# Kernel tuning notes

Hardware: AMD Instinct MI355X
Metric: run time of the kernel (lower is better)

## Reference

```python
import jax, jax.numpy as jnp
import numpy as np

N, H, D = 65536, 8, 32      # n_points, num_heads, dim_per_head (h_dim)
CD = 3                      # coords_dim
NW = 3                      # num_w_per_dist
BS = 128                    # block_size
NH = 2                      # n_hashes


def layer_norm(x, g, b, eps=1e-5):
    mu = x.mean(-1, keepdims=True)
    var = ((x - mu) ** 2).mean(-1, keepdims=True)
    return (x - mu) * jax.lax.rsqrt(var + eps) * g + b


def hept_attn(q, k, v, pe, Wrpe):
    """HEPT-style LSH-sorted block-diagonal attention with relative-position kernel.
    q,k,v: (N,H,D); pe: (N,CD); Wrpe: (NW*(CD-1), H*D) (w_rpe.weight^T).
    score_ij = q_i.k_j/sqrt(D) - sum_r omega[h,r]*(p_i,r - p_j,r)^2 within LSH blocks.
    """
    # per-head, per-distance-dim nonnegative RPE weights derived from w_rpe.weight
    omega = (Wrpe.T.reshape(H, D, CD - 1, NW) ** 2).mean(axis=(1, 3))  # (H, CD-1)
    # E2LSH-style random projections of coordinates -> NH scalar hash codes
    proj = jax.random.normal(jax.random.key(42), (NH, CD), dtype=q.dtype)
    codes = pe @ proj.T  # (N, NH)
    scale = 1.0 / jnp.sqrt(jnp.asarray(D, q.dtype))
    nb = N // BS
    out = jnp.zeros((N, H * D), dtype=q.dtype)
    for r in range(NH):
        order = jnp.argsort(codes[:, r])
        inv = jnp.argsort(order)
        qs = q[order].reshape(nb, BS, H, D)
        ks = k[order].reshape(nb, BS, H, D)
        vs = v[order].reshape(nb, BS, H, D)
        ps = pe[order][:, : CD - 1].reshape(nb, BS, CD - 1)
        scores = jnp.einsum("bqhd,bkhd->bhqk", qs, ks) * scale      # (nb,H,BS,BS)
        diff2 = (ps[:, :, None, :] - ps[:, None, :, :]) ** 2        # (nb,BS,BS,CD-1)
        scores = scores - jnp.einsum("hr,bqkr->bhqk", omega, diff2)
        attn = jax.nn.softmax(scores, axis=-1)
        o = jnp.einsum("bhqk,bkhd->bqhd", attn, vs).reshape(N, H * D)
        out = out + o[inv]
    return out / NH


def setup_inputs() -> dict:
    key = jax.random.key(0)
    ks = jax.random.split(key, 16)
    s = 0.02
    return {
        "x": jax.random.normal(ks[0], (N, D), jnp.float32),
        "coords": jax.random.uniform(ks[1], (N, CD), jnp.float32),
        "g1": jnp.ones((D,), jnp.float32),
        "be1": jnp.zeros((D,), jnp.float32),
        "Wq": jax.random.normal(ks[2], (D, H * D), jnp.float32) * s,
        "Wk": jax.random.normal(ks[3], (D, H * D), jnp.float32) * s,
        "Wv": jax.random.normal(ks[4], (D, H * D), jnp.float32) * s,
        "Wrpe": jax.random.normal(ks[5], (NW * (CD - 1), H * D), jnp.float32) * s,
        "Wo": jax.random.normal(ks[6], (H * D, D), jnp.float32) * s,
        "bo": jnp.zeros((D,), jnp.float32),
        "g2": jnp.ones((D,), jnp.float32),
        "be2": jnp.zeros((D,), jnp.float32),
        "W1": jax.random.normal(ks[7], (D, D), jnp.float32) * s,
        "b1": jnp.zeros((D,), jnp.float32),
        "W2": jax.random.normal(ks[8], (D, D), jnp.float32) * s,
        "b2": jnp.zeros((D,), jnp.float32),
    }


def reference(x, coords, g1, be1, Wq, Wk, Wv, Wrpe, Wo, bo, g2, be2, W1, b1, W2, b2):
    # pe_type == 'none' -> pe = coords, x_pe = x (no additive PE)
    xn = layer_norm(x, g1, be1)
    q = (xn @ Wq).reshape(N, H, D)
    k = (xn @ Wk).reshape(N, H, D)
    v = (xn @ Wv).reshape(N, H, D)
    aggr = hept_attn(q, k, v, coords, Wrpe)
    x = x + aggr @ Wo + bo                       # residual (dropout = identity, eval)
    h = layer_norm(x, g2, be2)
    ff = jax.nn.relu(h @ W1 + b1) @ W2 + b2
    return x + ff
```

## Files before the change

### kernel.cpp

```cpp
#include <hip/hip_runtime.h>
#include <stdint.h>

typedef uint32_t u32;
typedef unsigned long long u64;
typedef unsigned short ushort;
typedef __attribute__((ext_vector_type(8))) short short8;
typedef __attribute__((ext_vector_type(4))) float f32x4;

#define NPTS 65536
#define HEADS 8
#define DIM 32
#define HD 256
#define BSZ 128
#define NBLK 512
#define SCALE_QK 0.17677669529663687f
#define LOG2E 1.4426950408889634f

__device__ __forceinline__ u32 rotl32(u32 v, int r){ return (v << r) | (v >> (32 - r)); }

__device__ void threefry2x32_0_42(u32 x0, u32 x1, u32& o0, u32& o1){
  const u32 ks0 = 0u, ks1 = 42u;
  const u32 ks2 = ks0 ^ ks1 ^ 0x1BD11BDAu;
  x0 += ks0; x1 += ks1;
#define TF_RND(r) { x0 += x1; x1 = rotl32(x1, (r)); x1 ^= x0; }
  TF_RND(13) TF_RND(15) TF_RND(26) TF_RND(6)
  x0 += ks1; x1 += ks2 + 1u;
  TF_RND(17) TF_RND(29) TF_RND(16) TF_RND(24)
  x0 += ks2; x1 += ks0 + 2u;
  TF_RND(13) TF_RND(15) TF_RND(26) TF_RND(6)
  x0 += ks0; x1 += ks1 + 3u;
  TF_RND(17) TF_RND(29) TF_RND(16) TF_RND(24)
  x0 += ks1; x1 += ks2 + 4u;
  TF_RND(13) TF_RND(15) TF_RND(26) TF_RND(6)
  x0 += ks2; x1 += ks0 + 5u;
#undef TF_RND
  o0 = x0; o1 = x1;
}

__device__ float erfinv_xla_f32(float x){
  float w = -log1pf(-x * x);
  float p;
  if (w < 5.0f){
    w = w - 2.5f;
    p =            2.81022636e-08f;
    p = fmaf(p, w, 3.43273939e-07f);
    p = fmaf(p, w, -3.5233877e-06f);
    p = fmaf(p, w, -4.39150654e-06f);
    p = fmaf(p, w,  0.00021858087f);
    p = fmaf(p, w, -0.00125372503f);
    p = fmaf(p, w, -0.00417768164f);
    p = fmaf(p, w,  0.246640727f);
    p = fmaf(p, w,  1.50140941f);
  } else {
    w = sqrtf(w) - 3.0f;
    p =            -0.000200214257f;
    p = fmaf(p, w,  0.000100950558f);
    p = fmaf(p, w,  0.00134934322f);
    p = fmaf(p, w, -0.00367342844f);
    p = fmaf(p, w,  0.00573950773f);
    p = fmaf(p, w, -0.0076224613f);
    p = fmaf(p, w,  0.00943887047f);
    p = fmaf(p, w,  1.00167406f);
    p = fmaf(p, w,  2.83297682f);
  }
  return p * x;
}

__device__ float jax_normal_from_bits(u32 bits){
  float f = __uint_as_float((bits >> 9) | 0x3f800000u) - 1.0f;
  const float mn = -0.99999994f;
  float v = fmaf(f, 2.0f, mn);
  v = fmaxf(mn, v);
  return 1.41421356237309505f * erfinv_xla_f32(v);
}

__device__ __forceinline__ ushort f2bf(float f){
  union { __bf16 b; ushort u; } cv;
  cv.b = (__bf16)f;
  return cv.u;
}

__global__ __launch_bounds__(1024) void k_sort2048(const float* __restrict__ coords,
                                                   const float* __restrict__ Wrpe,
                                                   const float* __restrict__ x,
                                                   const float* __restrict__ g1,
                                                   const float* __restrict__ be1,
                                                   float* __restrict__ omega,
                                                   ushort* __restrict__ xn,
                                                   u64* __restrict__ A0, u64* __restrict__ A1){
  __shared__ u64 sh[2048];
  int t = threadIdx.x;
  int bb = blockIdx.x;
  int r = (bb >= 32);
  u64* A = r ? A1 : A0;
  int base = (bb & 31) * 2048;

  {
    int gt = bb*1024 + t;
    const float4* xp = (const float4*)(x + (size_t)gt*32);
    float mu = 0.f, s2 = 0.f;
    #pragma unroll
    for (int c4 = 0; c4 < 8; c4++){
      float4 f = xp[c4];
      mu += f.x + f.y + f.z + f.w;
      s2 = fmaf(f.x,f.x, fmaf(f.y,f.y, fmaf(f.z,f.z, fmaf(f.w,f.w, s2))));
    }
    mu *= (1.0f/32.0f);
    float var = fmaf(-mu, mu, s2*(1.0f/32.0f));
    float rs = rsqrtf(var + 1e-5f);
    #pragma unroll
    for (int c4 = 0; c4 < 8; c4++){
      float4 f = xp[c4];
      u32 w0 = (u32)f2bf((f.x-mu)*rs*g1[c4*4+0] + be1[c4*4+0])
             | ((u32)f2bf((f.y-mu)*rs*g1[c4*4+1] + be1[c4*4+1]) << 16);
      u32 w1 = (u32)f2bf((f.z-mu)*rs*g1[c4*4+2] + be1[c4*4+2])
             | ((u32)f2bf((f.w-mu)*rs*g1[c4*4+3] + be1[c4*4+3]) << 16);
      *(uint2*)&xn[(size_t)gt*32 + c4*4] = make_uint2(w0, w1);
    }
  }

  float pr[3];
  #pragma unroll
  for (int j = 0; j < 3; j++){
    u32 a, b;
    threefry2x32_0_42((u32)j, (u32)(j + 3), a, b);
    pr[j] = jax_normal_from_bits(r ? b : a);
  }
  #pragma unroll
  for (int half = 0; half < 2; half++){
    int idx = base + t + half*1024;
    float c0 = coords[idx*3+0], c1 = coords[idx*3+1], c2 = coords[idx*3+2];
    float code = fmaf(c2, pr[2], fmaf(c1, pr[1], c0*pr[0]));
    u32 u = __float_as_uint(code);
    u32 key = (u & 0x80000000u) ? ~u : (u | 0x80000000u);
    sh[t + half*1024] = ((u64)key << 32) | (u64)(u32)idx;
  }
  __syncthreads();
  for (int k = 2; k <= 2048; k <<= 1){
    for (int j = k >> 1; j > 0; j >>= 1){
      int idx = ((t & ~(j-1)) << 1) | (t & (j-1));
      int par = idx | j;
      bool up = ((idx & k) == 0);
      u64 a = sh[idx], b = sh[par];
      if ((a > b) == up){ sh[idx] = b; sh[par] = a; }
      __syncthreads();
    }
  }
  A[base + t] = sh[t];
  A[base + t + 1024] = sh[t + 1024];

  if (bb == 0 && t < 16){
    int h = t >> 1, rr = t & 1;
    float s = 0.f;
    for (int wi = 0; wi < 3; wi++)
      for (int d = 0; d < 32; d++){
        float w = Wrpe[(rr*3 + wi)*HD + h*32 + d];
        s = fmaf(w, w, s);
      }
    omega[t] = s * (1.0f/96.0f);
  }
}

template<int NRG>
__global__ void k_merge2(const u64* __restrict__ s0, const u64* __restrict__ s1,
                         u64* __restrict__ d0, u64* __restrict__ d1, int lgL){
  int gb = blockIdx.x;
  const u64* src = (gb < 256) ? s0 : s1;
  u64*       dst = (gb < 256) ? d0 : d1;
  int g = (gb & 255) * 256 + threadIdx.x;
  int L = 1 << lgL;
  u64 e = src[g];
  int myrun = (g >> lgL) & (NRG - 1);
  int gbase = g & ~(NRG*L - 1);
  int pos = g & (L - 1);
  #pragma unroll
  for (int o = 0; o < NRG; o++){
    if (o == myrun) continue;
    const u64* run = src + gbase + o*L;
    int lo = 0, hi = L;
    while (lo < hi){
      int mid = (lo + hi) >> 1;
      if (run[mid] < e) lo = mid + 1; else hi = mid;
    }
    pos += lo;
  }
  dst[gbase + pos] = e;
}

__global__ __launch_bounds__(256, 4) void k_attn(const u64* __restrict__ s0,
    const u64* __restrict__ s1,
    const ushort* __restrict__ xn, const float* __restrict__ coords,
    const float* __restrict__ Wq, const float* __restrict__ Wk, const float* __restrict__ Wv,
    const float* __restrict__ omega, ushort* __restrict__ ag0, ushort* __restrict__ ag1){
  __shared__ __align__(16) char smem[38400];
  ushort* Xs = (ushort*)(smem + 0);
  ushort* Wt = (ushort*)(smem + 10240);
  ushort* Ps = (ushort*)(smem + 0);
  ushort* Ks = (ushort*)(smem + 17920);
  ushort* Vt = (ushort*)(smem + 28160);
  int*    gq_s = (int*)(smem + 36864);
  float2* ps_s = (float2*)(smem + 37376);
  ushort* Qs = Xs;

  const int bid = blockIdx.x;
  const int h = bid >> 10;
  const int b = (bid >> 1) & 511;
  const int r = bid & 1;
  const u64* sorted = r ? s1 : s0;
  ushort* aggr = r ? ag1 : ag0;

  const int t = threadIdx.x;
  const int w = t >> 6, l = t & 63, lg = l >> 4, lc = l & 15;
  const int R = w * 32;

  if (t < 128){
    int gp = (int)(u32)(sorted[b*BSZ + t] & 0xffffffffull);
    gq_s[t] = gp;
    float2 pc; pc.x = coords[gp*3+0]; pc.y = coords[gp*3+1];
    ps_s[t] = pc;
    const uint4* xr = (const uint4*)(xn + (size_t)gp*32);
    #pragma unroll
    for (int q4 = 0; q4 < 4; q4++)
      *(uint4*)&Xs[t*40 + q4*8] = xr[q4];
  } else {
    int tt = t - 128;
    #pragma unroll
    for (int e = 0; e < 24; e++){
      int flat = tt + e*128;
      int c  = (flat >> 5) & 31;
      int dl = flat & 31;
      const float* Wm = (e < 8) ? Wq : (e < 16) ? Wk : Wv;
      int m = e >> 3;
      float wv_ = Wm[c*HD + h*32 + dl];
      if (e < 8) wv_ *= SCALE_QK * LOG2E;
      Wt[(m*32 + dl)*40 + c] = f2bf(wv_);
    }
  }
  __syncthreads();

  {
    short8 a0 = *(const short8*)&Xs[(R      + lc)*40 + lg*8];
    short8 a1 = *(const short8*)&Xs[(R + 16 + lc)*40 + lg*8];
    short8 wq0 = *(const short8*)&Wt[(     lc)*40 + lg*8];
    short8 wq1 = *(const short8*)&Wt[(16 + lc)*40 + lg*8];
    f32x4 qtc[2][2];
    qtc[0][0] = __builtin_amdgcn_mfma_f32_16x16x32_bf16(wq0, a0, (f32x4){0.f,0.f,0.f,0.f}, 0, 0, 0);
    qtc[0][1] = __builtin_amdgcn_mfma_f32_16x16x32_bf16(wq0, a1, (f32x4){0.f,0.f,0.f,0.f}, 0, 0, 0);
    qtc[1][0] = __builtin_amdgcn_mfma_f32_16x16x32_bf16(wq1, a0, (f32x4){0.f,0.f,0.f,0.f}, 0, 0, 0);
    qtc[1][1] = __builtin_amdgcn_mfma_f32_16x16x32_bf16(wq1, a1, (f32x4){0.f,0.f,0.f,0.f}, 0, 0, 0);
    #pragma unroll
    for (int ct = 2; ct < 6; ct++){
      short8 bb = *(const short8*)&Wt[(ct*16 + lc)*40 + lg*8];
      f32x4 d0 = __builtin_amdgcn_mfma_f32_16x16x32_bf16(a0, bb, (f32x4){0.f,0.f,0.f,0.f}, 0, 0, 0);
      f32x4 d1 = __builtin_amdgcn_mfma_f32_16x16x32_bf16(a1, bb, (f32x4){0.f,0.f,0.f,0.f}, 0, 0, 0);
      #pragma unroll
      for (int i = 0; i < 4; i++){
        int r0 = R + lg*4 + i, r1 = r0 + 16;
        if (ct < 4){
          Ks[r0*40 + (ct-2)*16 + lc] = f2bf(d0[i]);
          Ks[r1*40 + (ct-2)*16 + lc] = f2bf(d1[i]);
        } else {
          Vt[((ct-4)*16 + lc)*136 + r0] = f2bf(d0[i]);
          Vt[((ct-4)*16 + lc)*136 + r1] = f2bf(d1[i]);
        }
      }
    }
    #pragma unroll
    for (int qt = 0; qt < 2; qt++)
      #pragma unroll
      for (int dt = 0; dt < 2; dt++){
        u32 w0 = (u32)f2bf(qtc[dt][qt][0]) | ((u32)f2bf(qtc[dt][qt][1]) << 16);
        u32 w1 = (u32)f2bf(qtc[dt][qt][2]) | ((u32)f2bf(qtc[dt][qt][3]) << 16);
        *(uint2*)&Qs[(R + qt*16 + lc)*40 + dt*16 + lg*4] = make_uint2(w0, w1);
      }
  }
  __syncthreads();

  short8 bq[2];
  bq[0] = *(const short8*)&Qs[(R      + lc)*40 + lg*8];
  bq[1] = *(const short8*)&Qs[(R + 16 + lc)*40 + lg*8];

  const float om0 = omega[h*2+0] * LOG2E, om1 = omega[h*2+1] * LOG2E;
  short8 bAug[2];
  #pragma unroll
  for (int qt = 0; qt < 2; qt++){
    float2 pq = ps_s[R + qt*16 + lc];
    u32 wrd[4];
    wrd[0] = (lg == 0) ? ((u32)f2bf(2.0f*om0*pq.x) | ((u32)f2bf(2.0f*om1*pq.y) << 16)) : 0u;
    wrd[1] = (lg == 0) ? (u32)f2bf(1.0f) : 0u;
    wrd[2] = 0u; wrd[3] = 0u;
    bAug[qt] = *(short8*)&wrd[0];
  }

  f32x4 acc[2][8];
  #pragma unroll
  for (int kt = 0; kt < 8; kt++){
    short8 ak = *(const short8*)&Ks[(kt*16 + lc)*40 + lg*8];
    float2 pk = ps_s[kt*16 + lc];
    float nK = -fmaf(om0, pk.x*pk.x, om1*(pk.y*pk.y));
    u32 wrd[4];
    wrd[0] = (lg == 0) ? ((u32)f2bf(pk.x) | ((u32)f2bf(pk.y) << 16)) : 0u;
    wrd[1] = (lg == 0) ? (u32)f2bf(nK) : 0u;
    wrd[2] = 0u; wrd[3] = 0u;
    short8 aAug = *(short8*)&wrd[0];
    acc[0][kt] = __builtin_amdgcn_mfma_f32_16x16x32_bf16(ak, bq[0], (f32x4){0.f,0.f,0.f,0.f}, 0, 0, 0);
    acc[1][kt] = __builtin_amdgcn_mfma_f32_16x16x32_bf16(ak, bq[1], (f32x4){0.f,0.f,0.f,0.f}, 0, 0, 0);
    acc[0][kt] = __builtin_amdgcn_mfma_f32_16x16x32_bf16(aAug, bAug[0], acc[0][kt], 0, 0, 0);
    acc[1][kt] = __builtin_amdgcn_mfma_f32_16x16x32_bf16(aAug, bAug[1], acc[1][kt], 0, 0, 0);
  }

  float lr[2] = {0.f, 0.f};
  #pragma unroll
  for (int qt = 0; qt < 2; qt++)
    #pragma unroll
    for (int kt = 0; kt < 8; kt++)
      #pragma unroll
      for (int i = 0; i < 4; i++){
        float e = exp2f(acc[qt][kt][i]);
        acc[qt][kt][i] = e;
        lr[qt] += e;
      }
  #pragma unroll
  for (int qt = 0; qt < 2; qt++){
    float s = lr[qt];
    s += __shfl_xor(s, 16);
    s += __shfl_xor(s, 32);
    lr[qt] = 0.5f / s;
  }

  short8 av[4][2];
  #pragma unroll
  for (int cc = 0; cc < 4; cc++)
    #pragma unroll
    for (int dt = 0; dt < 2; dt++)
      av[cc][dt] = *(const short8*)&Vt[(dt*16 + lc)*136 + cc*32 + lg*8];

  __syncthreads();

  ushort* Psw = Ps + w*16*136;
  f32x4 oT[2][2];
  #pragma unroll
  for (int dt = 0; dt < 2; dt++)
    #pragma unroll
    for (int qt = 0; qt < 2; qt++) oT[dt][qt] = (f32x4){0.f,0.f,0.f,0.f};

  #pragma unroll
  for (int qt = 0; qt < 2; qt++){
    asm volatile("s_waitcnt lgkmcnt(0)" ::: "memory");
    __builtin_amdgcn_sched_barrier(0);
    #pragma unroll
    for (int kt = 0; kt < 8; kt++){
      u32 p0 = (u32)f2bf(acc[qt][kt][0]) | ((u32)f2bf(acc[qt][kt][1]) << 16);
      u32 p1 = (u32)f2bf(acc[qt][kt][2]) | ((u32)f2bf(acc[qt][kt][3]) << 16);
      *(uint2*)&Psw[lc*136 + kt*16 + lg*4] = make_uint2(p0, p1);
    }
    asm volatile("s_waitcnt lgkmcnt(0)" ::: "memory");
    __builtin_amdgcn_sched_barrier(0);
    __builtin_amdgcn_s_setprio(1);
    #pragma unroll
    for (int cc = 0; cc < 4; cc++){
      short8 bp = *(const short8*)&Psw[lc*136 + cc*32 + lg*8];
      oT[0][qt] = __builtin_amdgcn_mfma_f32_16x16x32_bf16(av[cc][0], bp, oT[0][qt], 0, 0, 0);
      oT[1][qt] = __builtin_amdgcn_mfma_f32_16x16x32_bf16(av[cc][1], bp, oT[1][qt], 0, 0, 0);
    }
    __builtin_amdgcn_s_setprio(0);
  }

  #pragma unroll
  for (int qt = 0; qt < 2; qt++){
    int g = gq_s[R + qt*16 + lc];
    float lrq = lr[qt];
    ushort* dst = aggr + (size_t)g*HD + h*32;
    #pragma unroll
    for (int dt = 0; dt < 2; dt++){
      u32 w0 = (u32)f2bf(oT[dt][qt][0]*lrq) | ((u32)f2bf(oT[dt][qt][1]*lrq) << 16);
      u32 w1 = (u32)f2bf(oT[dt][qt][2]*lrq) | ((u32)f2bf(oT[dt][qt][3]*lrq) << 16);
      *(uint2*)&dst[dt*16 + lg*4] = make_uint2(w0, w1);
    }
  }
}

__global__ __launch_bounds__(256) void k_out(const float* __restrict__ x,
    const ushort* __restrict__ ag0, const ushort* __restrict__ ag1,
    const float* __restrict__ Wo, const float* __restrict__ bo,
    const float* __restrict__ g2, const float* __restrict__ be2,
    const float* __restrict__ W1, const float* __restrict__ b1,
    const float* __restrict__ W2, const float* __restrict__ b2,
    float* __restrict__ out){
  __shared__ ushort Wot[32*264];
  __shared__ ushort W1t[32*40];
  __shared__ ushort W2t[32*40];
  __shared__ ushort Bnc[4][16*40];
  int t = threadIdx.x;
  #pragma unroll
  for (int e = 0; e < 32; e++){
    int flat = t + e*256;
    int k = flat >> 5, col = flat & 31;
    Wot[col*264 + k] = f2bf(Wo[flat]);
  }
  #pragma unroll
  for (int e = 0; e < 4; e++){
    int flat = t + e*256;
    int k = flat >> 5, col = flat & 31;
    W1t[col*40 + k] = f2bf(W1[flat]);
    W2t[col*40 + k] = f2bf(W2[flat]);
  }
  __syncthreads();

  const int w = t >> 6, l = t & 63, lg = l >> 4, lc = l & 15;
  const int r0 = blockIdx.x*64 + w*16;

  f32x4 acc[2];
  acc[0] = (f32x4){0.f,0.f,0.f,0.f};
  acc[1] = (f32x4){0.f,0.f,0.f,0.f};
  #pragma unroll
  for (int ks = 0; ks < 8; ks++){
    short8 a0 = *(const short8*)(ag0 + (size_t)(r0+lc)*256 + ks*32 + lg*8);
    short8 a1 = *(const short8*)(ag1 + (size_t)(r0+lc)*256 + ks*32 + lg*8);
    #pragma unroll
    for (int ct = 0; ct < 2; ct++){
      short8 bb = *(const short8*)&Wot[(ct*16 + lc)*264 + ks*32 + lg*8];
      acc[ct] = __builtin_amdgcn_mfma_f32_16x16x32_bf16(a0, bb, acc[ct], 0, 0, 0);
      acc[ct] = __builtin_amdgcn_mfma_f32_16x16x32_bf16(a1, bb, acc[ct], 0, 0, 0);
    }
  }
  float x2v[2][4];
  #pragma unroll
  for (int ct = 0; ct < 2; ct++){
    int col = ct*16 + lc;
    float bov = bo[col];
    #pragma unroll
    for (int i = 0; i < 4; i++){
      int row = r0 + lg*4 + i;
      x2v[ct][i] = x[row*32 + col] + acc[ct][i] + bov;
    }
  }

  float g2v[2], be2v[2], b1v[2], b2v[2];
  #pragma unroll
  for (int ct = 0; ct < 2; ct++){
    int col = ct*16 + lc;
    g2v[ct] = g2[col]; be2v[ct] = be2[col]; b1v[ct] = b1[col]; b2v[ct] = b2[col];
  }
  ushort* B = &Bnc[w][0];
  #pragma unroll
  for (int i = 0; i < 4; i++){
    float m = x2v[0][i] + x2v[1][i];
    m += __shfl_xor(m, 1); m += __shfl_xor(m, 2);
    m += __shfl_xor(m, 4); m += __shfl_xor(m, 8);
    float mu = m * (1.0f/32.0f);
    float d0 = x2v[0][i] - mu, d1 = x2v[1][i] - mu;
    float v = fmaf(d0, d0, d1*d1);
    v += __shfl_xor(v, 1); v += __shfl_xor(v, 2);
    v += __shfl_xor(v, 4); v += __shfl_xor(v, 8);
    float rs = rsqrtf(v * (1.0f/32.0f) + 1e-5f);
    B[(lg*4 + i)*40 +      lc] = f2bf(d0 * rs * g2v[0] + be2v[0]);
    B[(lg*4 + i)*40 + 16 + lc] = f2bf(d1 * rs * g2v[1] + be2v[1]);
  }
  asm volatile("s_waitcnt lgkmcnt(0)" ::: "memory");
  __builtin_amdgcn_sched_barrier(0);

  short8 ha = *(const short8*)&B[lc*40 + lg*8];
  f32x4 f1[2];
  #pragma unroll
  for (int ct = 0; ct < 2; ct++){
    short8 bb = *(const short8*)&W1t[(ct*16 + lc)*40 + lg*8];
    f1[ct] = __builtin_amdgcn_mfma_f32_16x16x32_bf16(ha, bb, (f32x4){0.f,0.f,0.f,0.f}, 0, 0, 0);
  }
  asm volatile("s_waitcnt lgkmcnt(0)" ::: "memory");
  __builtin_amdgcn_sched_barrier(0);
  #pragma unroll
  for (int ct = 0; ct < 2; ct++)
    #pragma unroll
    for (int i = 0; i < 4; i++)
      B[(lg*4 + i)*40 + ct*16 + lc] = f2bf(fmaxf(f1[ct][i] + b1v[ct], 0.f));
  asm volatile("s_waitcnt lgkmcnt(0)" ::: "memory");
  __builtin_amdgcn_sched_barrier(0);

  short8 ta = *(const short8*)&B[lc*40 + lg*8];
  #pragma unroll
  for (int ct = 0; ct < 2; ct++){
    short8 bb = *(const short8*)&W2t[(ct*16 + lc)*40 + lg*8];
    f32x4 f2 = __builtin_amdgcn_mfma_f32_16x16x32_bf16(ta, bb, (f32x4){0.f,0.f,0.f,0.f}, 0, 0, 0);
    int col = ct*16 + lc;
    #pragma unroll
    for (int i = 0; i < 4; i++){
      int row = r0 + lg*4 + i;
      out[row*32 + col] = x2v[ct][i] + f2[i] + b2v[ct];
    }
  }
}

extern "C" void kernel_launch(void* const* d_in, const int* in_sizes, int n_in,
                              void* d_out, int out_size, void* d_ws, size_t ws_size,
                              hipStream_t stream) {
  (void)in_sizes; (void)n_in; (void)out_size; (void)ws_size;
  const float* x      = (const float*)d_in[0];
  const float* coords = (const float*)d_in[1];
  const float* g1     = (const float*)d_in[2];
  const float* be1    = (const float*)d_in[3];
  const float* Wq     = (const float*)d_in[4];
  const float* Wk     = (const float*)d_in[5];
  const float* Wv     = (const float*)d_in[6];
  const float* Wrpe   = (const float*)d_in[7];
  const float* Wo     = (const float*)d_in[8];
  const float* bo     = (const float*)d_in[9];
  const float* g2     = (const float*)d_in[10];
  const float* be2    = (const float*)d_in[11];
  const float* W1     = (const float*)d_in[12];
  const float* b1     = (const float*)d_in[13];
  const float* W2     = (const float*)d_in[14];
  const float* b2     = (const float*)d_in[15];
  float* out = (float*)d_out;

  char* ws = (char*)d_ws;
  ushort* ag0   = (ushort*)(ws + 0);
  ushort* ag1   = (ushort*)(ws + 33554432);
  ushort* xn    = (ushort*)(ws + 67108864);
  u64*   keyA0  = (u64*)  (ws + 71303168);
  u64*   keyA1  = (u64*)  (ws + 71827456);
  u64*   keyB0  = (u64*)  (ws + 72351744);
  u64*   keyB1  = (u64*)  (ws + 72876032);
  float* omega  = (float*)(ws + 73400320);

  k_sort2048<<<64, 1024, 0, stream>>>(coords, Wrpe, x, g1, be1, omega, xn, keyA0, keyA1);
  k_merge2<4><<<512, 256, 0, stream>>>(keyA0, keyA1, keyB0, keyB1, 11);
  k_merge2<4><<<512, 256, 0, stream>>>(keyB0, keyB1, keyA0, keyA1, 13);
  k_merge2<2><<<512, 256, 0, stream>>>(keyA0, keyA1, keyB0, keyB1, 15);

  k_attn<<<NBLK*HEADS*2, 256, 0, stream>>>(keyB0, keyB1, xn, coords,
                                           Wq, Wk, Wv, omega, ag0, ag1);

  k_out<<<NPTS/64, 256, 0, stream>>>(x, ag0, ag1, Wo, bo, g2, be2, W1, b1, W2, b2, out);
}
```

Before: 144.3 us.

## Shrink bitonic sort tiles to 1024 and compute K via transposed MFMA

The initial bitonic sort now sorts 1024-key tiles with 512-thread blocks on 128 blocks instead of 2048-key tiles on 64 blocks. The merge passes are re-parameterised so that three radix-4 merges cover the larger number of runs. Separately, the attention kernel now computes K with the weight as the A operand, the same way as Q. This lets K be written to shared memory with packed 8-byte stores instead of scattered 2-byte stores, and V stores are also packed. The aim is better GPU occupancy in the sort and fewer LDS store instructions in the QKV projection, in exchange for a final merge that is 4-way instead of 2-way.

```diff
diff --git a/kernel.cpp b/kernel.cpp
--- a/kernel.cpp
+++ b/kernel.cpp
@@ -80,23 +80,23 @@
   return cv.u;
 }
 
-__global__ __launch_bounds__(1024) void k_sort2048(const float* __restrict__ coords,
-                                                   const float* __restrict__ Wrpe,
-                                                   const float* __restrict__ x,
-                                                   const float* __restrict__ g1,
-                                                   const float* __restrict__ be1,
-                                                   float* __restrict__ omega,
-                                                   ushort* __restrict__ xn,
-                                                   u64* __restrict__ A0, u64* __restrict__ A1){
-  __shared__ u64 sh[2048];
+__global__ __launch_bounds__(512) void k_sort1024(const float* __restrict__ coords,
+                                                  const float* __restrict__ Wrpe,
+                                                  const float* __restrict__ x,
+                                                  const float* __restrict__ g1,
+                                                  const float* __restrict__ be1,
+                                                  float* __restrict__ omega,
+                                                  ushort* __restrict__ xn,
+                                                  u64* __restrict__ A0, u64* __restrict__ A1){
+  __shared__ u64 sh[1024];
   int t = threadIdx.x;
   int bb = blockIdx.x;
-  int r = (bb >= 32);
+  int r = (bb >= 64);
   u64* A = r ? A1 : A0;
-  int base = (bb & 31) * 2048;
+  int base = (bb & 63) * 1024;
 
   {
-    int gt = bb*1024 + t;
+    int gt = bb*512 + t;
     const float4* xp = (const float4*)(x + (size_t)gt*32);
     float mu = 0.f, s2 = 0.f;
     #pragma unroll
@@ -128,15 +128,15 @@
   }
   #pragma unroll
   for (int half = 0; half < 2; half++){
-    int idx = base + t + half*1024;
+    int idx = base + t + half*512;
     float c0 = coords[idx*3+0], c1 = coords[idx*3+1], c2 = coords[idx*3+2];
     float code = fmaf(c2, pr[2], fmaf(c1, pr[1], c0*pr[0]));
     u32 u = __float_as_uint(code);
     u32 key = (u & 0x80000000u) ? ~u : (u | 0x80000000u);
-    sh[t + half*1024] = ((u64)key << 32) | (u64)(u32)idx;
+    sh[t + half*512] = ((u64)key << 32) | (u64)(u32)idx;
   }
   __syncthreads();
-  for (int k = 2; k <= 2048; k <<= 1){
+  for (int k = 2; k <= 1024; k <<= 1){
     for (int j = k >> 1; j > 0; j >>= 1){
       int idx = ((t & ~(j-1)) << 1) | (t & (j-1));
       int par = idx | j;
@@ -147,7 +147,7 @@
     }
   }
   A[base + t] = sh[t];
-  A[base + t + 1024] = sh[t + 1024];
+  A[base + t + 512] = sh[t + 512];
 
   if (bb == 0 && t < 16){
     int h = t >> 1, rr = t & 1;
@@ -241,38 +241,40 @@
   {
     short8 a0 = *(const short8*)&Xs[(R      + lc)*40 + lg*8];
     short8 a1 = *(const short8*)&Xs[(R + 16 + lc)*40 + lg*8];
-    short8 wq0 = *(const short8*)&Wt[(     lc)*40 + lg*8];
-    short8 wq1 = *(const short8*)&Wt[(16 + lc)*40 + lg*8];
-    f32x4 qtc[2][2];
-    qtc[0][0] = __builtin_amdgcn_mfma_f32_16x16x32_bf16(wq0, a0, (f32x4){0.f,0.f,0.f,0.f}, 0, 0, 0);
-    qtc[0][1] = __builtin_amdgcn_mfma_f32_16x16x32_bf16(wq0, a1, (f32x4){0.f,0.f,0.f,0.f}, 0, 0, 0);
-    qtc[1][0] = __builtin_amdgcn_mfma_f32_16x16x32_bf16(wq1, a0, (f32x4){0.f,0.f,0.f,0.f}, 0, 0, 0);
-    qtc[1][1] = __builtin_amdgcn_mfma_f32_16x16x32_bf16(wq1, a1, (f32x4){0.f,0.f,0.f,0.f}, 0, 0, 0);
-    #pragma unroll
-    for (int ct = 2; ct < 6; ct++){
-      short8 bb = *(const short8*)&Wt[(ct*16 + lc)*40 + lg*8];
-      f32x4 d0 = __builtin_amdgcn_mfma_f32_16x16x32_bf16(a0, bb, (f32x4){0.f,0.f,0.f,0.f}, 0, 0, 0);
-      f32x4 d1 = __builtin_amdgcn_mfma_f32_16x16x32_bf16(a1, bb, (f32x4){0.f,0.f,0.f,0.f}, 0, 0, 0);
-      #pragma unroll
-      for (int i = 0; i < 4; i++){
-        int r0 = R + lg*4 + i, r1 = r0 + 16;
-        if (ct < 4){
-          Ks[r0*40 + (ct-2)*16 + lc] = f2bf(d0[i]);
-          Ks[r1*40 + (ct-2)*16 + lc] = f2bf(d1[i]);
-        } else {
-          Vt[((ct-4)*16 + lc)*136 + r0] = f2bf(d0[i]);
-          Vt[((ct-4)*16 + lc)*136 + r1] = f2bf(d1[i]);
-        }
-      }
-    }
-    #pragma unroll
-    for (int qt = 0; qt < 2; qt++)
-      #pragma unroll
-      for (int dt = 0; dt < 2; dt++){
-        u32 w0 = (u32)f2bf(qtc[dt][qt][0]) | ((u32)f2bf(qtc[dt][qt][1]) << 16);
-        u32 w1 = (u32)f2bf(qtc[dt][qt][2]) | ((u32)f2bf(qtc[dt][qt][3]) << 16);
-        *(uint2*)&Qs[(R + qt*16 + lc)*40 + dt*16 + lg*4] = make_uint2(w0, w1);
-      }
+    const f32x4 z = (f32x4){0.f,0.f,0.f,0.f};
+    #pragma unroll
+    for (int dt = 0; dt < 2; dt++){
+      short8 wq = *(const short8*)&Wt[(     dt*16 + lc)*40 + lg*8];
+      short8 wk = *(const short8*)&Wt[(32 + dt*16 + lc)*40 + lg*8];
+      f32x4 q0 = __builtin_amdgcn_mfma_f32_16x16x32_bf16(wq, a0, z, 0, 0, 0);
+      f32x4 q1 = __builtin_amdgcn_mfma_f32_16x16x32_bf16(wq, a1, z, 0, 0, 0);
+      f32x4 k0 = __builtin_amdgcn_mfma_f32_16x16x32_bf16(wk, a0, z, 0, 0, 0);
+      f32x4 k1 = __builtin_amdgcn_mfma_f32_16x16x32_bf16(wk, a1, z, 0, 0, 0);
+      u32 qw0 = (u32)f2bf(q0[0]) | ((u32)f2bf(q0[1]) << 16);
+      u32 qw1 = (u32)f2bf(q0[2]) | ((u32)f2bf(q0[3]) << 16);
+      *(uint2*)&Qs[(R      + lc)*40 + dt*16 + lg*4] = make_uint2(qw0, qw1);
+      qw0 = (u32)f2bf(q1[0]) | ((u32)f2bf(q1[1]) << 16);
+      qw1 = (u32)f2bf(q1[2]) | ((u32)f2bf(q1[3]) << 16);
+      *(uint2*)&Qs[(R + 16 + lc)*40 + dt*16 + lg*4] = make_uint2(qw0, qw1);
+      u32 kw0 = (u32)f2bf(k0[0]) | ((u32)f2bf(k0[1]) << 16);
+      u32 kw1 = (u32)f2bf(k0[2]) | ((u32)f2bf(k0[3]) << 16);
+      *(uint2*)&Ks[(R      + lc)*40 + dt*16 + lg*4] = make_uint2(kw0, kw1);
+      kw0 = (u32)f2bf(k1[0]) | ((u32)f2bf(k1[1]) << 16);
+      kw1 = (u32)f2bf(k1[2]) | ((u32)f2bf(k1[3]) << 16);
+      *(uint2*)&Ks[(R + 16 + lc)*40 + dt*16 + lg*4] = make_uint2(kw0, kw1);
+    }
+    #pragma unroll
+    for (int vt = 0; vt < 2; vt++){
+      short8 wv = *(const short8*)&Wt[(64 + vt*16 + lc)*40 + lg*8];
+      f32x4 v0 = __builtin_amdgcn_mfma_f32_16x16x32_bf16(a0, wv, z, 0, 0, 0);
+      f32x4 v1 = __builtin_amdgcn_mfma_f32_16x16x32_bf16(a1, wv, z, 0, 0, 0);
+      u32 vw0 = (u32)f2bf(v0[0]) | ((u32)f2bf(v0[1]) << 16);
+      u32 vw1 = (u32)f2bf(v0[2]) | ((u32)f2bf(v0[3]) << 16);
+      *(uint2*)&Vt[(vt*16 + lc)*136 + R      + lg*4] = make_uint2(vw0, vw1);
+      vw0 = (u32)f2bf(v1[0]) | ((u32)f2bf(v1[1]) << 16);
+      vw1 = (u32)f2bf(v1[2]) | ((u32)f2bf(v1[3]) << 16);
+      *(uint2*)&Vt[(vt*16 + lc)*136 + R + 16 + lg*4] = make_uint2(vw0, vw1);
+    }
   }
   __syncthreads();
 
@@ -523,10 +525,10 @@
   u64*   keyB1  = (u64*)  (ws + 72876032);
   float* omega  = (float*)(ws + 73400320);
 
-  k_sort2048<<<64, 1024, 0, stream>>>(coords, Wrpe, x, g1, be1, omega, xn, keyA0, keyA1);
-  k_merge2<4><<<512, 256, 0, stream>>>(keyA0, keyA1, keyB0, keyB1, 11);
-  k_merge2<4><<<512, 256, 0, stream>>>(keyB0, keyB1, keyA0, keyA1, 13);
-  k_merge2<2><<<512, 256, 0, stream>>>(keyA0, keyA1, keyB0, keyB1, 15);
+  k_sort1024<<<128, 512, 0, stream>>>(coords, Wrpe, x, g1, be1, omega, xn, keyA0, keyA1);
+  k_merge2<4><<<512, 256, 0, stream>>>(keyA0, keyA1, keyB0, keyB1, 10);
+  k_merge2<4><<<512, 256, 0, stream>>>(keyB0, keyB1, keyA0, keyA1, 12);
+  k_merge2<4><<<512, 256, 0, stream>>>(keyA0, keyA1, keyB0, keyB1, 14);
 
   k_attn<<<NBLK*HEADS*2, 256, 0, stream>>>(keyB0, keyB1, xn, coords,
                                            Wq, Wk, Wv, omega, ag0, ag1);
```

Measured after the change: 139.1 us. 3.6% less time.
